# Performance work log

Hardware: AMD Instinct MI355X
Metric: run time of the kernel (lower is better)

The kernel has to match this reference:

```python
import jax, jax.numpy as jnp
import numpy as np

# 256 graphs x 1024 nodes, 64 channels, 4.19M edges (avg degree 16)
B, N, C, E = 256, 1024, 64, 4194304
RATIO = 0.5
K = 512  # ceil(RATIO * N), fixed per-graph keep count


def setup_inputs() -> dict:
    key = jax.random.key(0)
    k1, k2, k3, k4, k5, k6 = jax.random.split(key, 6)
    x = jax.random.normal(k1, (B * N, C), jnp.float32)
    w = jax.random.normal(k2, (1, C), jnp.float32) / np.sqrt(C)  # score_layer.weight
    b = jnp.zeros((1,), jnp.float32)                              # score_layer.bias
    # edges sampled within each graph so filter_adj semantics are realistic
    g = jax.random.randint(k3, (E,), 0, B)
    src = jax.random.randint(k4, (E,), 0, N)
    dst = jax.random.randint(k5, (E,), 0, N)
    edge_index = jnp.stack([g * N + src, g * N + dst]).astype(jnp.int32)
    edge_attr = jax.random.normal(k6, (E,), jnp.float32)
    batch = jnp.repeat(jnp.arange(B, dtype=jnp.int32), N)  # nondecreasing graph ids
    return {"x": x, "w": w, "b": b, "edge_index": edge_index,
            "edge_attr": edge_attr, "batch": batch}


def reference(x, w, b, edge_index, edge_attr, batch):
    # scores = Linear(x).squeeze() / ||W||  (bias also divided, as in source)
    scores = (x @ w.T + b)[:, 0] / jnp.linalg.norm(w)  # [B*N]
    # per-graph ratio top-k (equal-size graphs -> dense [B, N] top_k, fixed K)
    _, top_idx = jax.lax.top_k(scores.reshape(B, N), K)          # [B, K] local ids
    perm = (top_idx + (jnp.arange(B) * N)[:, None]).reshape(-1)  # [B*K] global ids
    x_p = x[perm]          # gather surviving node features
    batch_p = batch[perm]
    # filter_adj: relabel kept nodes 0..B*K-1, drop edges touching removed nodes.
    # For jit-able static shapes we keep [2, E] and mask dropped edges to -1
    # instead of compacting (mask returned for downstream compaction).
    new_idx = jnp.full((B * N,), -1, jnp.int32).at[perm].set(
        jnp.arange(B * K, dtype=jnp.int32))
    r = new_idx[edge_index[0]]
    c = new_idx[edge_index[1]]
    mask = (r >= 0) & (c >= 0)
    ei = jnp.where(mask, jnp.stack([r, c]), -1)
    ea = jnp.where(mask, edge_attr, jnp.zeros((), edge_attr.dtype))
    return x_p, ei, ea, batch_p, scores, perm, mask
```

## Files before the change

### kernel.cpp

```cpp
#include <hip/hip_runtime.h>
#include <math.h>

#define BGRAPHS 256
#define NNODES  1024
#define CCH     64
#define NEDGE   4194304
#define KKEEP   512

typedef unsigned long long u64;
typedef unsigned int u32;
typedef unsigned short u16;
typedef float  f32x4 __attribute__((ext_vector_type(4)));
typedef int    i32x4 __attribute__((ext_vector_type(4)));

#define OFF_XP   0
#define OFF_EI0  8388608
#define OFF_EI1  (8388608 + NEDGE)
#define OFF_EA   16777216
#define OFF_BP   20971520
#define OFF_SC   21102592
#define OFF_PM   21364736
#define OFF_MSK  21495808

__global__ __launch_bounds__(256) void score_kernel(
    const float* __restrict__ x, const float* __restrict__ w,
    const float* __restrict__ bias, float* __restrict__ sco)
{
    __shared__ float s_w[CCH];
    const int tid = threadIdx.x;
    if (tid < CCH) s_w[tid] = w[tid];
    __syncthreads();

    double n2 = 0.0;
    #pragma unroll
    for (int k = 0; k < CCH; ++k) { double v = (double)s_w[k]; n2 += v * v; }
    const float nrm = (float)sqrt(n2);
    const float bv = bias[0];

    const int node = blockIdx.x * 256 + tid;
    const f32x4* x4 = (const f32x4*)x;
    double acc = 0.0;
    #pragma unroll
    for (int k = 0; k < 16; ++k) {
        f32x4 xv = x4[node * 16 + k];
        acc += (double)xv.x * (double)s_w[4 * k + 0];
        acc += (double)xv.y * (double)s_w[4 * k + 1];
        acc += (double)xv.z * (double)s_w[4 * k + 2];
        acc += (double)xv.w * (double)s_w[4 * k + 3];
    }
    sco[node] = ((float)acc + bv) / nrm;
}

__global__ __launch_bounds__(1024) void sort_kernel(
    const float* __restrict__ sco, const int* __restrict__ batch,
    float* __restrict__ pmo, float* __restrict__ bpo,
    u16* __restrict__ table16, u16* __restrict__ src16)
{
    __shared__ u64 s_key[NNODES];
    const int b = blockIdx.x;
    const int tid = threadIdx.x;
    const int node = b * NNODES + tid;

    const float score = sco[node];
    u32 u = __float_as_uint(score);
    u32 mu = u ^ (u32)(((int)u >> 31) | 0x80000000);
    s_key[tid] = ((u64)(~mu) << 32) | (u32)tid;

    for (int k = 2; k <= NNODES; k <<= 1) {
        for (int j = k >> 1; j > 0; j >>= 1) {
            __syncthreads();
            int ixj = tid ^ j;
            if (ixj > tid) {
                u64 a = s_key[tid], c = s_key[ixj];
                bool up = ((tid & k) == 0);
                if ((a > c) == up) { s_key[tid] = c; s_key[ixj] = a; }
            }
        }
    }
    __syncthreads();

    const int lidx = (int)(u32)s_key[tid];
    const int g = b * NNODES + lidx;
    if (tid < KKEEP) {
        pmo[b * KKEEP + tid] = (float)g;
        bpo[b * KKEEP + tid] = (float)batch[g];
        table16[g] = (u16)tid;
        src16[b * KKEEP + tid] = (u16)lidx;
    } else {
        table16[g] = 0xFFFFu;
    }
}

__global__ __launch_bounds__(256) void gather_kernel(
    const float* __restrict__ x, const u16* __restrict__ src16,
    float* __restrict__ xp)
{
    const int elem = blockIdx.x * 256 + threadIdx.x;
    const int row = elem >> 4;
    const int col = elem & 15;
    const int b = row >> 9;
    const int src = (int)src16[row];
    const f32x4* x4 = (const f32x4*)x;
    ((f32x4*)xp)[elem] = x4[((b << 10) + src) * 16 + col];
}

__global__ __launch_bounds__(256) void edge_kernel(
    const int* __restrict__ ei, const float* __restrict__ ea,
    const u16* __restrict__ table16,
    float* __restrict__ ei0o, float* __restrict__ ei1o,
    float* __restrict__ eao, float* __restrict__ msk)
{
    const int gid = blockIdx.x * 256 + threadIdx.x;
    const i32x4* s4p = (const i32x4*)ei;
    const i32x4* d4p = (const i32x4*)(ei + NEDGE);
    const f32x4* a4p = (const f32x4*)ea;

    i32x4 s4 = __builtin_nontemporal_load(&s4p[gid]);
    i32x4 d4 = __builtin_nontemporal_load(&d4p[gid]);
    f32x4 a4 = __builtin_nontemporal_load(&a4p[gid]);
    f32x4 r4, c4, o4, m4;

#define PROC(comp)                                                 \
    {                                                              \
        u16 vs = table16[s4.comp];                                 \
        u16 vd = table16[d4.comp];                                 \
        int m = (vs != 0xFFFFu) && (vd != 0xFFFFu);                \
        int r = ((s4.comp >> 10) << 9) + (int)vs;                  \
        int c = ((d4.comp >> 10) << 9) + (int)vd;                  \
        r4.comp = m ? (float)r : -1.0f;                            \
        c4.comp = m ? (float)c : -1.0f;                            \
        o4.comp = m ? a4.comp : 0.0f;                              \
        m4.comp = (float)m;                                        \
    }
    PROC(x) PROC(y) PROC(z) PROC(w)
#undef PROC

    __builtin_nontemporal_store(r4, &((f32x4*)ei0o)[gid]);
    __builtin_nontemporal_store(c4, &((f32x4*)ei1o)[gid]);
    __builtin_nontemporal_store(o4, &((f32x4*)eao)[gid]);
    __builtin_nontemporal_store(m4, &((f32x4*)msk)[gid]);
}

extern "C" void kernel_launch(void* const* d_in, const int* in_sizes, int n_in,
                              void* d_out, int out_size, void* d_ws, size_t ws_size,
                              hipStream_t stream) {
    const float* x          = (const float*)d_in[0];
    const float* w          = (const float*)d_in[1];
    const float* bias       = (const float*)d_in[2];
    const int*   edge_index = (const int*)d_in[3];
    const float* edge_attr  = (const float*)d_in[4];
    const int*   batch      = (const int*)d_in[5];

    float* out = (float*)d_out;
    float* xp   = out + OFF_XP;
    float* ei0o = out + OFF_EI0;
    float* ei1o = out + OFF_EI1;
    float* eao  = out + OFF_EA;
    float* bpo  = out + OFF_BP;
    float* sco  = out + OFF_SC;
    float* pmo  = out + OFF_PM;
    float* msk  = out + OFF_MSK;

    u16* table16 = (u16*)d_ws;
    u16* src16   = (u16*)d_ws + BGRAPHS * NNODES;

    score_kernel<<<BGRAPHS * NNODES / 256, 256, 0, stream>>>(x, w, bias, sco);
    sort_kernel<<<BGRAPHS, 1024, 0, stream>>>(sco, batch, pmo, bpo, table16, src16);
    gather_kernel<<<BGRAPHS * KKEEP * 16 / 256, 256, 0, stream>>>(x, src16, xp);
    edge_kernel<<<NEDGE / 4 / 256, 256, 0, stream>>>(edge_index, edge_attr, table16,
                                                     ei0o, ei1o, eao, msk);
}
```

Measured before the change: 251.6 us.

## Use wave shuffles in bitonic sort and fuse edge filter with feature gather

The bitonic sort now does every compare-exchange stage with stride 32 or less inside a 64-wide wavefront using shuffles, which removes most of the LDS traffic and block-wide barriers. Only the strides of 64 and above still go through shared memory. The gather and edge-filter kernels are merged into one launch whose blocks branch by index, saving a launch and letting the two memory-bound jobs overlap. Each edge thread now handles two float4 groups, which gives more loads in flight at the cost of higher register use.

```diff
diff --git a/kernel.cpp b/kernel.cpp
--- a/kernel.cpp
+++ b/kernel.cpp
@@ -21,6 +21,9 @@
 #define OFF_SC   21102592
 #define OFF_PM   21364736
 #define OFF_MSK  21495808
+
+#define EDGE_BLOCKS   2048
+#define GATHER_BLOCKS 8192
 
 __global__ __launch_bounds__(256) void score_kernel(
     const float* __restrict__ x, const float* __restrict__ w,
@@ -51,6 +54,14 @@
     sco[node] = ((float)acc + bv) / nrm;
 }
 
+__device__ __forceinline__ u64 cmpex(u64 key, int j, bool dir, int tid) {
+    u64 o = (u64)__shfl_xor((long long)key, j, 64);
+    bool lower = ((tid & j) == 0);
+    u64 mn = key < o ? key : o;
+    u64 mx = key < o ? o : key;
+    return (dir == lower) ? mn : mx;
+}
+
 __global__ __launch_bounds__(1024) void sort_kernel(
     const float* __restrict__ sco, const int* __restrict__ batch,
     float* __restrict__ pmo, float* __restrict__ bpo,
@@ -64,22 +75,35 @@
     const float score = sco[node];
     u32 u = __float_as_uint(score);
     u32 mu = u ^ (u32)(((int)u >> 31) | 0x80000000);
-    s_key[tid] = ((u64)(~mu) << 32) | (u32)tid;
-
-    for (int k = 2; k <= NNODES; k <<= 1) {
-        for (int j = k >> 1; j > 0; j >>= 1) {
+    u64 key = ((u64)(~mu) << 32) | (u32)tid;
+
+    #pragma unroll
+    for (int k = 2; k <= 64; k <<= 1) {
+        bool dir = ((tid & k) == 0);
+        for (int j = k >> 1; j > 0; j >>= 1)
+            key = cmpex(key, j, dir, tid);
+    }
+    s_key[tid] = key;
+
+    for (int k = 128; k <= NNODES; k <<= 1) {
+        bool dir = ((tid & k) == 0);
+        for (int j = k >> 1; j >= 64; j >>= 1) {
             __syncthreads();
             int ixj = tid ^ j;
             if (ixj > tid) {
                 u64 a = s_key[tid], c = s_key[ixj];
-                bool up = ((tid & k) == 0);
-                if ((a > c) == up) { s_key[tid] = c; s_key[ixj] = a; }
+                if ((a > c) == dir) { s_key[tid] = c; s_key[ixj] = a; }
             }
         }
-    }
-    __syncthreads();
-
-    const int lidx = (int)(u32)s_key[tid];
+        __syncthreads();
+        key = s_key[tid];
+        #pragma unroll
+        for (int j = 32; j > 0; j >>= 1)
+            key = cmpex(key, j, dir, tid);
+        s_key[tid] = key;
+    }
+
+    const int lidx = (int)(u32)key;
     const int g = b * NNODES + lidx;
     if (tid < KKEEP) {
         pmo[b * KKEEP + tid] = (float)g;
@@ -91,54 +115,79 @@
     }
 }
 
-__global__ __launch_bounds__(256) void gather_kernel(
+__global__ __launch_bounds__(256) void edge_gather_kernel(
+    const int* __restrict__ ei, const float* __restrict__ ea,
+    const u16* __restrict__ table16,
     const float* __restrict__ x, const u16* __restrict__ src16,
+    float* __restrict__ ei0o, float* __restrict__ ei1o,
+    float* __restrict__ eao, float* __restrict__ msk,
     float* __restrict__ xp)
 {
-    const int elem = blockIdx.x * 256 + threadIdx.x;
-    const int row = elem >> 4;
-    const int col = elem & 15;
-    const int b = row >> 9;
-    const int src = (int)src16[row];
-    const f32x4* x4 = (const f32x4*)x;
-    ((f32x4*)xp)[elem] = x4[((b << 10) + src) * 16 + col];
-}
-
-__global__ __launch_bounds__(256) void edge_kernel(
-    const int* __restrict__ ei, const float* __restrict__ ea,
-    const u16* __restrict__ table16,
-    float* __restrict__ ei0o, float* __restrict__ ei1o,
-    float* __restrict__ eao, float* __restrict__ msk)
-{
-    const int gid = blockIdx.x * 256 + threadIdx.x;
-    const i32x4* s4p = (const i32x4*)ei;
-    const i32x4* d4p = (const i32x4*)(ei + NEDGE);
-    const f32x4* a4p = (const f32x4*)ea;
-
-    i32x4 s4 = __builtin_nontemporal_load(&s4p[gid]);
-    i32x4 d4 = __builtin_nontemporal_load(&d4p[gid]);
-    f32x4 a4 = __builtin_nontemporal_load(&a4p[gid]);
-    f32x4 r4, c4, o4, m4;
-
-#define PROC(comp)                                                 \
-    {                                                              \
-        u16 vs = table16[s4.comp];                                 \
-        u16 vd = table16[d4.comp];                                 \
-        int m = (vs != 0xFFFFu) && (vd != 0xFFFFu);                \
-        int r = ((s4.comp >> 10) << 9) + (int)vs;                  \
-        int c = ((d4.comp >> 10) << 9) + (int)vd;                  \
-        r4.comp = m ? (float)r : -1.0f;                            \
-        c4.comp = m ? (float)c : -1.0f;                            \
-        o4.comp = m ? a4.comp : 0.0f;                              \
-        m4.comp = (float)m;                                        \
-    }
-    PROC(x) PROC(y) PROC(z) PROC(w)
-#undef PROC
-
-    __builtin_nontemporal_store(r4, &((f32x4*)ei0o)[gid]);
-    __builtin_nontemporal_store(c4, &((f32x4*)ei1o)[gid]);
-    __builtin_nontemporal_store(o4, &((f32x4*)eao)[gid]);
-    __builtin_nontemporal_store(m4, &((f32x4*)msk)[gid]);
+    const int tid = threadIdx.x;
+    if (blockIdx.x < EDGE_BLOCKS) {
+        const int i0 = blockIdx.x * 512 + tid;
+        const int i1 = i0 + 256;
+        const i32x4* s4p = (const i32x4*)ei;
+        const i32x4* d4p = (const i32x4*)(ei + NEDGE);
+        const f32x4* a4p = (const f32x4*)ea;
+
+        i32x4 sA = __builtin_nontemporal_load(&s4p[i0]);
+        i32x4 sB = __builtin_nontemporal_load(&s4p[i1]);
+        i32x4 dA = __builtin_nontemporal_load(&d4p[i0]);
+        i32x4 dB = __builtin_nontemporal_load(&d4p[i1]);
+        f32x4 aA = __builtin_nontemporal_load(&a4p[i0]);
+        f32x4 aB = __builtin_nontemporal_load(&a4p[i1]);
+
+        u16 vsA[4], vdA[4], vsB[4], vdB[4];
+        #pragma unroll
+        for (int q = 0; q < 4; ++q) vsA[q] = table16[((const int*)&sA)[q]];
+        #pragma unroll
+        for (int q = 0; q < 4; ++q) vdA[q] = table16[((const int*)&dA)[q]];
+        #pragma unroll
+        for (int q = 0; q < 4; ++q) vsB[q] = table16[((const int*)&sB)[q]];
+        #pragma unroll
+        for (int q = 0; q < 4; ++q) vdB[q] = table16[((const int*)&dB)[q]];
+
+        f32x4 rA, cA, oA, mA, rB, cB, oB, mB;
+        #pragma unroll
+        for (int q = 0; q < 4; ++q) {
+            {
+                int m = (vsA[q] != 0xFFFFu) && (vdA[q] != 0xFFFFu);
+                int r = ((((const int*)&sA)[q] >> 10) << 9) + (int)vsA[q];
+                int c = ((((const int*)&dA)[q] >> 10) << 9) + (int)vdA[q];
+                ((float*)&rA)[q] = m ? (float)r : -1.0f;
+                ((float*)&cA)[q] = m ? (float)c : -1.0f;
+                ((float*)&oA)[q] = m ? ((const float*)&aA)[q] : 0.0f;
+                ((float*)&mA)[q] = (float)m;
+            }
+            {
+                int m = (vsB[q] != 0xFFFFu) && (vdB[q] != 0xFFFFu);
+                int r = ((((const int*)&sB)[q] >> 10) << 9) + (int)vsB[q];
+                int c = ((((const int*)&dB)[q] >> 10) << 9) + (int)vdB[q];
+                ((float*)&rB)[q] = m ? (float)r : -1.0f;
+                ((float*)&cB)[q] = m ? (float)c : -1.0f;
+                ((float*)&oB)[q] = m ? ((const float*)&aB)[q] : 0.0f;
+                ((float*)&mB)[q] = (float)m;
+            }
+        }
+
+        __builtin_nontemporal_store(rA, &((f32x4*)ei0o)[i0]);
+        __builtin_nontemporal_store(rB, &((f32x4*)ei0o)[i1]);
+        __builtin_nontemporal_store(cA, &((f32x4*)ei1o)[i0]);
+        __builtin_nontemporal_store(cB, &((f32x4*)ei1o)[i1]);
+        __builtin_nontemporal_store(oA, &((f32x4*)eao)[i0]);
+        __builtin_nontemporal_store(oB, &((f32x4*)eao)[i1]);
+        __builtin_nontemporal_store(mA, &((f32x4*)msk)[i0]);
+        __builtin_nontemporal_store(mB, &((f32x4*)msk)[i1]);
+    } else {
+        const int elem = (blockIdx.x - EDGE_BLOCKS) * 256 + tid;
+        const int row = elem >> 4;
+        const int col = elem & 15;
+        const int b = row >> 9;
+        const int src = (int)src16[row];
+        const f32x4* x4 = (const f32x4*)x;
+        ((f32x4*)xp)[elem] = x4[((b << 10) + src) * 16 + col];
+    }
 }
 
 extern "C" void kernel_launch(void* const* d_in, const int* in_sizes, int n_in,
@@ -166,7 +215,6 @@
 
     score_kernel<<<BGRAPHS * NNODES / 256, 256, 0, stream>>>(x, w, bias, sco);
     sort_kernel<<<BGRAPHS, 1024, 0, stream>>>(sco, batch, pmo, bpo, table16, src16);
-    gather_kernel<<<BGRAPHS * KKEEP * 16 / 256, 256, 0, stream>>>(x, src16, xp);
-    edge_kernel<<<NEDGE / 4 / 256, 256, 0, stream>>>(edge_index, edge_attr, table16,
-                                                     ei0o, ei1o, eao, msk);
-}
+    edge_gather_kernel<<<EDGE_BLOCKS + GATHER_BLOCKS, 256, 0, stream>>>(
+        edge_index, edge_attr, table16, x, src16, ei0o, ei1o, eao, msk, xp);
+}
```

New measurement: 244.8 us. 1.03x faster.
